# Optimization experiments

Measured on AMD Instinct MI355X. Metric: run time of the kernel, lower is better.

The kernel has to match this reference:

```python
import jax, jax.numpy as jnp
import numpy as np

V, B, NP, NJ = 5, 32, 20, 17
NB = 16
ND = 128
POSE_MIN_DEPTH, POSE_MAX_DEPTH = 2000.0, 8000.0
POSE_SIGMA = 100.0
KS = 11
HIDDEN_ROUGH, HIDDEN = 1024, 1024
BONES = np.array([[0,1],[0,2],[1,3],[2,4],[5,6],[5,7],[7,9],[6,8],[8,10],[5,11],[6,12],[11,12],[11,13],[13,15],[12,14],[14,16]], dtype=np.int32)


def setup_inputs() -> dict:
    key = jax.random.key(0)
    ks = jax.random.split(key, 12)
    wh = jnp.array([1920.0, 1080.0], jnp.float32)
    kpts = jax.random.uniform(ks[0], (V, B, NP, NJ, 2), jnp.float32) * wh
    pose_vis = jnp.ones((V, B, NP), jnp.float32)
    joint_vis = (jax.random.uniform(ks[1], (V, B, NP, NJ)) > 0.15).astype(jnp.float32)
    gt_pose_depths = jax.random.uniform(ks[2], (B, NP), jnp.float32, 2000.0, 8000.0)
    gt_joint_depths = jax.random.uniform(ks[3], (B, NP, NJ), jnp.float32, -100.0, 100.0)
    angles = np.linspace(-0.3, 0.3, V)
    Rs = np.stack([np.array([[np.cos(a), 0.0, np.sin(a)], [0.0, 1.0, 0.0], [-np.sin(a), 0.0, np.cos(a)]], dtype=np.float32) for a in angles])
    cam_R = jnp.broadcast_to(jnp.asarray(Rs)[:, None], (V, B, 3, 3))
    tvec = np.zeros((V, 3), np.float32); tvec[:, 0] = np.linspace(-500.0, 500.0, V)
    cam_T = jnp.broadcast_to(jnp.asarray(tvec)[:, None], (V, B, 3))
    cam_f = jnp.full((V, B, 2), 1400.0, jnp.float32)
    cam_c = jnp.broadcast_to(jnp.array([960.0, 540.0], jnp.float32), (V, B, 2))
    image_wh = jnp.broadcast_to(jnp.array([1920.0, 1080.0], jnp.float32), (V, B, 2))
    num_persons = jax.random.randint(ks[4], (V, B), 10, NP + 1, jnp.int32)
    Wr1 = jax.random.normal(ks[5], (HIDDEN_ROUGH, NJ * 2)) * 0.02
    br1 = jnp.zeros((HIDDEN_ROUGH,), jnp.float32)
    Wr2 = jax.random.normal(ks[6], (NJ, HIDDEN_ROUGH)) * 0.02
    br2 = jnp.zeros((NJ,), jnp.float32)
    Wc1 = jax.random.normal(ks[7], (HIDDEN, NJ + NB, 3)) * 0.02
    bc1 = jnp.zeros((HIDDEN,), jnp.float32)
    Wc2 = jax.random.normal(ks[8], (1, HIDDEN, 3)) * 0.02
    bc2 = jnp.zeros((1,), jnp.float32)
    bones = jnp.asarray(BONES)
    return dict(kpts=kpts, pose_vis=pose_vis, joint_vis=joint_vis, gt_pose_depths=gt_pose_depths, gt_joint_depths=gt_joint_depths, cam_R=cam_R, cam_T=cam_T, cam_f=cam_f, cam_c=cam_c, image_wh=image_wh, num_persons=num_persons, Wr1=Wr1, br1=br1, Wr2=Wr2, br2=br2, Wc1=Wc1, bc1=bc1, Wc2=Wc2, bc2=bc2, bones=bones)


def _bone_len(p, bones):
    # p: [B, Np, Nj, D, 2] -> [B, Np, Nb, D]
    a = p[:, :, bones[:, 0]]
    b = p[:, :, bones[:, 1]]
    return jnp.sqrt(jnp.sum((a - b) ** 2, -1) + 1e-12)


def _conv1d(x, w, b):
    # x [N,C,L], w [O,I,3]
    y = jax.lax.conv_general_dilated(x, w, (1,), 'SAME', dimension_numbers=('NCH', 'OIH', 'NCH'))
    return y + b[None, :, None]


def _forward(kpts, joint_vis, cam_R, cam_T, cam_f, cam_c, image_wh, num_persons, Wr1, br1, Wr2, br2, Wc1, bc1, Wc2, bc2, bones):
    V_, B_, NP_, NJ_, _ = kpts.shape
    labels = jnp.arange(ND, dtype=jnp.float32) / (ND - 1) * (POSE_MAX_DEPTH - POSE_MIN_DEPTH) + POSE_MIN_DEPTH
    kt = kpts[0]  # target-view 2D poses [B,Np,Nj,2]
    # faithful to original indexing quirk: normalize all batches by batch-0 image size
    kn = kt / image_wh[0, 0][None, None, None, :]
    x = kn.reshape(B_ * NP_, NJ_ * 2)
    h = jax.nn.relu(x @ Wr1.T + br1)
    rough = (h @ Wr2.T + br2).reshape(B_, NP_, NJ_) * 1000.0
    rough = jax.lax.stop_gradient(rough)  # .detach() in original
    depths = labels[None, None, None, :] + rough[..., None]  # [B,Np,Nj,D]
    # back-project target 2D poses at every depth hypothesis
    R0, T0, f0, c0 = cam_R[0], cam_T[0], cam_f[0], cam_c[0]
    uvn = (kt - c0[:, None, None, :]) / f0[:, None, None, :]
    xy = uvn[..., None, :] * depths[..., None]
    cam_pts = jnp.concatenate([xy, depths[..., None]], -1)
    p3d = jnp.einsum('bji,bpkdj->bpkdi', R0, cam_pts) + T0[:, None, None, None, :]  # world [B,Np,Nj,D,3]

    scores = scores2 = boundings = boundings2 = None
    for rv in range(1, V_):
        Rr, Tr, fr, cr = cam_R[rv], cam_T[rv], cam_f[rv], cam_c[rv]
        xc = jnp.einsum('bij,bpkdj->bpkdi', Rr, p3d - Tr[:, None, None, None, :])
        p2t = xc[..., :2] / (xc[..., 2:3] + 1e-8) * fr[:, None, None, None, :] + cr[:, None, None, None, :]
        pr = kpts[rv]         # [B,Npr,Nj,2]
        vr = joint_vis[rv]    # [B,Npr,Nj]
        # pairwise dist over (target-person, ref-person) per joint/depth
        d = jnp.sum((p2t[:, :, None] - pr[:, None, :, :, None, :]) ** 2, -1)  # [B,Npt,Npr,Nj,D]
        w = vr[:, None, :, :, None]
        pdist = jnp.sum(d * w, 3) / (jnp.sum(w, 3) + 1e-8)  # [B,Npt,Npr,D]
        valid = jnp.arange(NP_)[None, None, :, None] < num_persons[rv][:, None, None, None]
        pdist = jnp.where(valid, pdist, 1e5)
        mm = jnp.argmin(pdist, 2)  # [B,Npt,D] nearest ref pose
        bidx = jnp.arange(B_)[:, None, None]
        matched = jnp.transpose(pr[bidx, mm], (0, 1, 3, 2, 4))  # [B,Npt,Nj,D,2]
        mvis = jnp.transpose(vr[bidx, mm], (0, 1, 3, 2))        # [B,Npt,Nj,D]
        mdist = jnp.sum((p2t - matched) ** 2, -1)
        score = jnp.exp(-jnp.sqrt(mdist + 1e-12) / POSE_SIGMA)  # panoptic branch
        score_bl = jnp.exp(-jnp.abs(_bone_len(matched, bones) - _bone_len(p2t, bones)) / 5.0)
        wimg = image_wh[rv][:, None, None, None, 0]
        himg = image_wh[rv][:, None, None, None, 1]
        inb = ((p2t[..., 0] >= 0) & (p2t[..., 1] >= 0) & (p2t[..., 0] <= wimg - 1) & (p2t[..., 1] <= himg - 1)).astype(score.dtype)
        bounding = inb * mvis
        bounding2 = jnp.broadcast_to(mvis[:, :, :1, :], score_bl.shape)
        if scores is None:
            scores, scores2 = score * bounding, score_bl * bounding2
            boundings, boundings2 = bounding, bounding2
        else:
            scores = scores + score * bounding
            scores2 = scores2 + score_bl * bounding2
            boundings = boundings + bounding
            boundings2 = boundings2 + bounding2
    psv = (scores / (boundings + 1e-8)).reshape(B_ * NP_, NJ_, ND)
    psv2 = (scores2 / (boundings2 + 1e-8)).reshape(B_ * NP_, NB, ND)
    xin = jnp.concatenate([psv, psv2], 1)  # [BN, Nj+Nb, D]
    hc = jax.nn.relu(_conv1d(xin, Wc1, bc1))
    logits = _conv1d(hc, Wc2, bc2)[:, 0, :]  # [BN, D]
    vol = jax.nn.softmax(logits, -1)
    # soft-argmax restricted to a window around the argmax
    pos = jnp.arange(ND, dtype=vol.dtype)
    idx = jnp.argmax(vol, -1)
    mask = (jnp.abs(pos[None, :] - idx[:, None].astype(vol.dtype)) <= KS // 2).astype(vol.dtype)
    mv = vol * mask
    mv = mv / (jnp.sum(mv, -1, keepdims=True) + 1e-8)
    pred_idx = jnp.sum(mv * pos, -1).reshape(B_, NP_)
    return pred_idx / (ND - 1) * (POSE_MAX_DEPTH - POSE_MIN_DEPTH) + POSE_MIN_DEPTH


def reference(kpts, pose_vis, joint_vis, gt_pose_depths, gt_joint_depths, cam_R, cam_T, cam_f, cam_c, image_wh, num_persons, Wr1, br1, Wr2, br2, Wc1, bc1, Wc2, bc2, bones):
    return _forward(kpts, joint_vis, cam_R, cam_T, cam_f, cam_c, image_wh, num_persons, Wr1, br1, Wr2, br2, Wc1, bc1, Wc2, bc2, bones)
```

## Files before the change

kernel.cpp:

```cpp
#include <hip/hip_runtime.h>
#include <math.h>

#define VV  5
#define BB  32
#define NPP 20
#define NJJ 17
#define NBB 16
#define NDD 128
#define HID 1024
#define KPITCH 128
#define KSTEPS 7
#define PRP 36
#define VRP 20
#define NCH 34
#define RGH_P 20
#define BASE_P 52
#define A_T_ELEMS (32 * KSTEPS * 64 * 8)
#define EPI_ELEMS (32 * 4 * 64 * 16)

typedef __attribute__((ext_vector_type(8))) short short8;
typedef __attribute__((ext_vector_type(16))) float float16;

static constexpr int BONE_A[NBB] = {0,0,1,2,5,5,7,6,8,5,6,11,11,13,12,14};
static constexpr int BONE_B[NBB] = {1,2,3,4,6,7,9,8,10,11,12,12,13,15,14,16};

__device__ __forceinline__ float warp_red_sum(float v) {
#pragma unroll
  for (int off = 32; off >= 1; off >>= 1) v += __shfl_xor(v, off, 64);
  return v;
}

__global__ __launch_bounds__(256) void prep_kernel(
    const float* __restrict__ Wc1, const float* __restrict__ Wc2,
    const float* __restrict__ bc1,
    unsigned short* __restrict__ A_hi, unsigned short* __restrict__ A_lo,
    float* __restrict__ epi) {
  int gidx = blockIdx.x * 256 + threadIdx.x;
  if (gidx < A_T_ELEMS) {
    int e = gidx & 7;
    int l = (gidx >> 3) & 63;
    int rest = gidx >> 9;
    int ks = rest % 7;
    int ot = rest / 7;
    int o = ot * 32 + (l & 31);
    int kk = ks * 16 + (l >> 5) * 8 + e;
    float x = (kk < 99) ? Wc1[o * 99 + kk] : 0.0f;
    unsigned int u = __float_as_uint(x);
    unsigned short hi = (unsigned short)(u >> 16);
    float xh = __uint_as_float((u >> 16) << 16);
    unsigned short lo = (unsigned short)(__float_as_uint(x - xh) >> 16);
    A_hi[gidx] = hi;
    A_lo[gidx] = lo;
  } else {
    int idx2 = gidx - A_T_ELEMS;
    if (idx2 < EPI_ELEMS) {
      int c = idx2 & 15;
      int l = (idx2 >> 4) & 63;
      int rb = (idx2 >> 10) & 3;
      int ot = idx2 >> 12;
      int base = ot * 32 + 4 * (l >> 5) + 8 * rb;
      epi[idx2] = (c < 12) ? Wc2[base * 3 + c] : bc1[base + (c - 12)];
    }
  }
}

__global__ __launch_bounds__(256) void pose_pre_kernel(
    const float* __restrict__ kpts, const float* __restrict__ cam_R,
    const float* __restrict__ cam_f, const float* __restrict__ cam_c,
    const float* __restrict__ image_wh,
    const float* __restrict__ Wr1, const float* __restrict__ br1,
    const float* __restrict__ Wr2, const float* __restrict__ br2,
    float* __restrict__ ws_rough, float* __restrict__ ws_base) {
  const int n = blockIdx.x;
  const int b = n / NPP;
  const int p = n % NPP;
  const int tid = threadIdx.x;
  const int wv = tid >> 6, ln = tid & 63;

  __shared__ float sh_x[NJJ * 2];
  __shared__ float sh_h[HID];

  if (tid < NJJ * 2) {
    int j = tid >> 1, c = tid & 1;
    float k = kpts[((size_t)(b * NPP + p)) * NJJ * 2 + j * 2 + c];
    sh_x[tid] = k / image_wh[c];
  }
  __syncthreads();

#pragma unroll
  for (int k = 0; k < 4; ++k) {
    int m = tid + k * 256;
    float acc = br1[m];
#pragma unroll
    for (int c = 0; c < NJJ * 2; ++c) acc = fmaf(Wr1[m * (NJJ * 2) + c], sh_x[c], acc);
    sh_h[m] = fmaxf(acc, 0.0f);
  }
  __syncthreads();

  for (int j = wv; j < NJJ; j += 4) {
    float part = 0.0f;
    for (int m = ln; m < HID; m += 64) part = fmaf(Wr2[j * HID + m], sh_h[m], part);
    part = warp_red_sum(part);
    if (ln == 0) ws_rough[(size_t)n * RGH_P + j] = (part + br2[j]) * 1000.0f;
  }

  if (tid < NJJ) {
    int j = tid;
    const float* R0 = cam_R + (size_t)b * 9;
    float c0x = cam_c[b * 2 + 0], c0y = cam_c[b * 2 + 1];
    float f0x = cam_f[b * 2 + 0], f0y = cam_f[b * 2 + 1];
    float kx = kpts[((size_t)(b * NPP + p)) * NJJ * 2 + j * 2 + 0];
    float ky = kpts[((size_t)(b * NPP + p)) * NJJ * 2 + j * 2 + 1];
    float ux = (kx - c0x) / f0x;
    float uy = (ky - c0y) / f0y;
#pragma unroll
    for (int i = 0; i < 3; ++i)
      ws_base[(size_t)n * BASE_P + j * 3 + i] =
          R0[0 * 3 + i] * ux + R0[1 * 3 + i] * uy + R0[2 * 3 + i];
  }
}

__global__ __launch_bounds__(256, 4) void pose_match_kernel(
    const float* __restrict__ kpts, const float* __restrict__ joint_vis,
    const float* __restrict__ cam_R, const float* __restrict__ cam_T,
    const float* __restrict__ cam_f, const float* __restrict__ cam_c,
    const float* __restrict__ image_wh, const int* __restrict__ num_persons,
    const float* __restrict__ ws_rough, const float* __restrict__ ws_base,
    float* __restrict__ ws_partial) {
  const int bid = blockIdx.x;
  const int n = bid >> 1;
  const int bh = bid & 1;
  const int b = n / NPP;
  const int tid = threadIdx.x;
  const int rvv = tid >> 6;
  const int d = bh * 64 + (tid & 63);

  __shared__ float sh_rough[NJJ];
  __shared__ float sh_base[NJJ][3];
  __shared__ __align__(16) float sh_pr[4][NPP][PRP];
  __shared__ __align__(16) float sh_vr[4][NPP][VRP];

  if (tid < NJJ) sh_rough[tid] = ws_rough[(size_t)n * RGH_P + tid];
  if (tid >= 64 && tid < 64 + NJJ * 3)
    ((float*)sh_base)[tid - 64] = ws_base[(size_t)n * BASE_P + (tid - 64)];

#pragma unroll
  for (int rr = 0; rr < 4; ++rr) {
    const float* prg = kpts + ((size_t)(rr + 1) * BB + b) * NPP * NJJ * 2;
    for (int idx = tid; idx < NPP * NJJ * 2; idx += 256)
      sh_pr[rr][idx / 34][idx % 34] = prg[idx];
    const float* vrg = joint_vis + ((size_t)(rr + 1) * BB + b) * NPP * NJJ;
    for (int idx = tid; idx < NPP * NJJ; idx += 256)
      sh_vr[rr][idx / 17][idx % 17] = vrg[idx];
  }
  if (tid < 4 * BB) {
    int rr = tid >> 5, q = tid & 31;
    if (q < NPP) {
      sh_pr[rr][q][34] = 0.0f; sh_pr[rr][q][35] = 0.0f;
      sh_vr[rr][q][17] = 0.0f; sh_vr[rr][q][18] = 0.0f; sh_vr[rr][q][19] = 0.0f;
    }
  }
  __syncthreads();

  {
    const int rv = rvv + 1;
    const int vb = rv * BB + b;
    const float* Rr = cam_R + (size_t)vb * 9;
    const float R00 = Rr[0], R01 = Rr[1], R02 = Rr[2];
    const float R10 = Rr[3], R11 = Rr[4], R12 = Rr[5];
    const float R20 = Rr[6], R21 = Rr[7], R22 = Rr[8];
    const float Trx = cam_T[vb * 3 + 0], Try = cam_T[vb * 3 + 1], Trz = cam_T[vb * 3 + 2];
    const float frx = cam_f[vb * 2 + 0], fry = cam_f[vb * 2 + 1];
    const float crx = cam_c[vb * 2 + 0], cry = cam_c[vb * 2 + 1];
    const float wmax = image_wh[vb * 2 + 0] - 1.0f;
    const float hmax = image_wh[vb * 2 + 1] - 1.0f;
    const int nprv = num_persons[vb];
    const float T0x = cam_T[b * 3 + 0], T0y = cam_T[b * 3 + 1], T0z = cam_T[b * 3 + 2];
    const float lab = ((float)d / 127.0f) * 6000.0f + 2000.0f;

    float px[NJJ], py[NJJ];
#pragma unroll
    for (int j = 0; j < NJJ; ++j) {
      float dep = lab + sh_rough[j];
      float p0 = fmaf(dep, sh_base[j][0], T0x);
      float p1 = fmaf(dep, sh_base[j][1], T0y);
      float p2 = fmaf(dep, sh_base[j][2], T0z);
      float q0 = p0 - Trx, q1 = p1 - Try, q2 = p2 - Trz;
      float xc0 = R00 * q0 + R01 * q1 + R02 * q2;
      float xc1 = R10 * q0 + R11 * q1 + R12 * q2;
      float xc2 = R20 * q0 + R21 * q1 + R22 * q2 + 1e-8f;
      px[j] = xc0 / xc2 * frx + crx;
      py[j] = xc1 / xc2 * fry + cry;
    }

    float best = 3.4e38f;
    int mm = 0;
#pragma unroll 1
    for (int q = 0; q < NPP; ++q) {
      const float4* pr4 = (const float4*)(&sh_pr[rvv][q][0]);
      const float4* vr4 = (const float4*)(&sh_vr[rvv][q][0]);
      float num = 0.0f, den = 0.0f;
#pragma unroll
      for (int g4 = 0; g4 < 4; ++g4) {
        float4 w  = vr4[g4];
        float4 pa = pr4[2 * g4 + 0];
        float4 pb = pr4[2 * g4 + 1];
        { float dx = px[4*g4+0] - pa.x, dy = py[4*g4+0] - pa.y; num = fmaf(w.x, dx*dx + dy*dy, num); den += w.x; }
        { float dx = px[4*g4+1] - pa.z, dy = py[4*g4+1] - pa.w; num = fmaf(w.y, dx*dx + dy*dy, num); den += w.y; }
        { float dx = px[4*g4+2] - pb.x, dy = py[4*g4+2] - pb.y; num = fmaf(w.z, dx*dx + dy*dy, num); den += w.z; }
        { float dx = px[4*g4+3] - pb.z, dy = py[4*g4+3] - pb.w; num = fmaf(w.w, dx*dx + dy*dy, num); den += w.w; }
      }
      {
        float w16 = sh_vr[rvv][q][16];
        float4 pc = pr4[8];
        float dx = px[16] - pc.x, dy = py[16] - pc.y;
        num = fmaf(w16, dx*dx + dy*dy, num); den += w16;
      }
      float pd = num / (den + 1e-8f);
      if (q >= nprv) pd = 100000.0f;
      if (pd < best) { best = pd; mm = q; }
    }

    float* pbase = ws_partial + (((size_t)n * NCH) * 4 + rvv) * 128 + d;
    unsigned int maskB = 0u;
#pragma unroll
    for (int j = 0; j < NJJ; ++j) {
      float mx = sh_pr[rvv][mm][j * 2 + 0];
      float my = sh_pr[rvv][mm][j * 2 + 1];
      float mv = sh_vr[rvv][mm][j];
      float dx = px[j] - mx, dy = py[j] - my;
      float sc = expf(-sqrtf(dx * dx + dy * dy + 1e-12f) / 100.0f);
      float inb = (px[j] >= 0.0f && py[j] >= 0.0f && px[j] <= wmax && py[j] <= hmax) ? 1.0f : 0.0f;
      float bd = inb * mv;
      pbase[j * 512] = sc * bd;
      maskB |= ((unsigned int)(bd != 0.0f)) << j;
    }
    float v0 = sh_vr[rvv][mm][0];
    maskB |= ((unsigned int)(v0 != 0.0f)) << 17;
#pragma unroll
    for (int nb = 0; nb < NBB; ++nb) {
      const int a = BONE_A[nb], c = BONE_B[nb];
      float ax = sh_pr[rvv][mm][a * 2 + 0], ay = sh_pr[rvv][mm][a * 2 + 1];
      float cx = sh_pr[rvv][mm][c * 2 + 0], cy = sh_pr[rvv][mm][c * 2 + 1];
      float dmx = ax - cx, dmy = ay - cy;
      float blm = sqrtf(dmx * dmx + dmy * dmy + 1e-12f);
      float dpx = px[a] - px[c], dpy = py[a] - py[c];
      float blp = sqrtf(dpx * dpx + dpy * dpy + 1e-12f);
      float scb = expf(-fabsf(blm - blp) / 5.0f);
      pbase[(NJJ + nb) * 512] = scb * v0;
    }
    *(unsigned int*)(pbase + 33 * 512) = maskB;
  }
}

__global__ __launch_bounds__(128) void reduce_kernel(
    const float* __restrict__ ws_partial, float* __restrict__ ws_xin) {
  const int n = blockIdx.x;
  const int t = threadIdx.x;
  const float* pb = ws_partial + ((size_t)n * NCH) * 4 * 128;
  float* xo = ws_xin + (size_t)n * (NJJ + NBB) * NDD;

  unsigned int m0 = __float_as_uint(pb[(33 * 4 + 0) * 128 + t]);
  unsigned int m1 = __float_as_uint(pb[(33 * 4 + 1) * 128 + t]);
  unsigned int m2 = __float_as_uint(pb[(33 * 4 + 2) * 128 + t]);
  unsigned int m3 = __float_as_uint(pb[(33 * 4 + 3) * 128 + t]);

#pragma unroll
  for (int i = 0; i < NJJ; ++i) {
    const float* a = pb + (i * 4) * 128 + t;
    float s = ((a[0] + a[128]) + a[256]) + a[384];
    int bj = ((m0 >> i) & 1) + ((m1 >> i) & 1) + ((m2 >> i) & 1) + ((m3 >> i) & 1);
    xo[i * NDD + t] = s / ((float)bj + 1e-8f);
  }
  int b2 = ((m0 >> 17) & 1) + ((m1 >> 17) & 1) + ((m2 >> 17) & 1) + ((m3 >> 17) & 1);
  float den2 = (float)b2 + 1e-8f;
#pragma unroll
  for (int nb = 0; nb < NBB; ++nb) {
    const float* a = pb + ((NJJ + nb) * 4) * 128 + t;
    float s = ((a[0] + a[128]) + a[256]) + a[384];
    xo[(NJJ + nb) * NDD + t] = s / den2;
  }
}

__global__ __launch_bounds__(512, 2) void conv_mfma_kernel(
    const float* __restrict__ ws_xin,
    const unsigned short* __restrict__ A_hi, const unsigned short* __restrict__ A_lo,
    const float* __restrict__ epi,
    const float* __restrict__ bc2, float* __restrict__ out) {
  const int n = blockIdx.x;
  const int tid = threadIdx.x;
  const int w = tid >> 6;
  const int l = tid & 63;
  const int lrow = l & 31;
  const int g = l >> 5;

  __shared__ __align__(16) unsigned short bT_hi[128 * KPITCH];
  __shared__ __align__(16) unsigned short bT_lo[128 * KPITCH];
  __shared__ float plg[3][8][NDD];
  __shared__ float sh_l[NDD];
  __shared__ float sh_e[NDD];
  __shared__ float sh_sc[2];

  for (int i = tid; i < 3 * 8 * NDD; i += 512) ((float*)plg)[i] = 0.0f;

  const float* xn = ws_xin + (size_t)n * (NJJ + NBB) * NDD;
  for (int idx = tid; idx < 64 * 128; idx += 512) {
    const int kp = (idx & 63) << 1;
    const int t  = idx >> 6;
    unsigned int hp = 0, lp = 0;
#pragma unroll
    for (int u = 0; u < 2; ++u) {
      const int kk = kp + u;
      float x = 0.0f;
      if (kk < 99) {
        int i3 = kk / 3;
        int k3 = kk - i3 * 3;
        int tt = t + k3 - 1;
        if (tt >= 0 && tt < 128) x = xn[i3 * NDD + tt];
      }
      unsigned int uu = __float_as_uint(x);
      unsigned int hi = uu >> 16;
      float xh = __uint_as_float(hi << 16);
      unsigned int lo = __float_as_uint(x - xh) >> 16;
      hp |= hi << (16 * u);
      lp |= lo << (16 * u);
    }
    const int e = t * KPITCH + (kp ^ ((t & 15) << 3));
    *(unsigned int*)(bT_hi + e) = hp;
    *(unsigned int*)(bT_lo + e) = lp;
  }
  __syncthreads();

#pragma unroll 1
  for (int otile = 0; otile < 4; ++otile) {
    const int otg = w * 4 + otile;

    short8 Ah[KSTEPS], Al[KSTEPS];
    {
      const short8* ahT = ((const short8*)A_hi) + (size_t)otg * KSTEPS * 64 + l;
      const short8* alT = ((const short8*)A_lo) + (size_t)otg * KSTEPS * 64 + l;
#pragma unroll
      for (int ks = 0; ks < KSTEPS; ++ks) {
        Ah[ks] = ahT[ks * 64];
        Al[ks] = alT[ks * 64];
      }
    }
    float w2f[48];
    float bcf[16];
#pragma unroll
    for (int rb = 0; rb < 4; ++rb) {
      const float4* ep = ((const float4*)epi) + ((size_t)(otg * 4 + rb) * 64 + l) * 4;
      float4 e0 = ep[0], e1 = ep[1], e2 = ep[2], e3 = ep[3];
      w2f[rb * 12 + 0] = e0.x;  w2f[rb * 12 + 1] = e0.y;  w2f[rb * 12 + 2] = e0.z;
      w2f[rb * 12 + 3] = e0.w;  w2f[rb * 12 + 4] = e1.x;  w2f[rb * 12 + 5] = e1.y;
      w2f[rb * 12 + 6] = e1.z;  w2f[rb * 12 + 7] = e1.w;  w2f[rb * 12 + 8] = e2.x;
      w2f[rb * 12 + 9] = e2.y;  w2f[rb * 12 + 10] = e2.z; w2f[rb * 12 + 11] = e2.w;
      bcf[rb * 4 + 0] = e3.x; bcf[rb * 4 + 1] = e3.y;
      bcf[rb * 4 + 2] = e3.z; bcf[rb * 4 + 3] = e3.w;
    }

#pragma unroll 1
    for (int ttile = 0; ttile < 4; ++ttile) {
      const int trow = ttile * 32 + lrow;
      const unsigned short* brh = bT_hi + trow * KPITCH;
      const unsigned short* brl = bT_lo + trow * KPITCH;
      const int sw = (trow & 15) << 3;

      float16 X, Y;
#pragma unroll
      for (int r = 0; r < 16; ++r) { X[r] = 0.0f; Y[r] = 0.0f; }

#pragma unroll
      for (int ks = 0; ks < KSTEPS; ++ks) {
        const int e = (ks * 16 + g * 8) ^ sw;
        short8 bh8 = *(const short8*)(brh + e);
        X = __builtin_amdgcn_mfma_f32_32x32x16_bf16(Ah[ks], bh8, X, 0, 0, 0);
        Y = __builtin_amdgcn_mfma_f32_32x32x16_bf16(Al[ks], bh8, Y, 0, 0, 0);
      }
#pragma unroll
      for (int ks = 0; ks < KSTEPS; ++ks) {
        const int e = (ks * 16 + g * 8) ^ sw;
        short8 bl8 = *(const short8*)(brl + e);
        if (ks & 1) Y = __builtin_amdgcn_mfma_f32_32x32x16_bf16(Ah[ks], bl8, Y, 0, 0, 0);
        else        X = __builtin_amdgcn_mfma_f32_32x32x16_bf16(Ah[ks], bl8, X, 0, 0, 0);
      }

      float sP = 0.0f, sC = 0.0f, sM = 0.0f;
#pragma unroll
      for (int r = 0; r < 16; ++r) {
        float h = fmaxf((X[r] + Y[r]) + bcf[(r >> 2) * 4 + (r & 3)], 0.0f);
        sP = fmaf(h, w2f[(r >> 2) * 12 + (r & 3) * 3 + 0], sP);
        sC = fmaf(h, w2f[(r >> 2) * 12 + (r & 3) * 3 + 1], sC);
        sM = fmaf(h, w2f[(r >> 2) * 12 + (r & 3) * 3 + 2], sM);
      }
      sP += __shfl_xor(sP, 32, 64);
      sC += __shfl_xor(sC, 32, 64);
      sM += __shfl_xor(sM, 32, 64);
      if (l < 32) {
        plg[0][w][trow] += sP;
        plg[1][w][trow] += sC;
        plg[2][w][trow] += sM;
      }
    }
  }
  __syncthreads();

  if (tid < NDD) {
    int t = tid;
    float lg = bc2[0];
#pragma unroll
    for (int ww = 0; ww < 8; ++ww) lg += plg[1][ww][t];
    if (t > 0) {
#pragma unroll
      for (int ww = 0; ww < 8; ++ww) lg += plg[0][ww][t - 1];
    }
    if (t < NDD - 1) {
#pragma unroll
      for (int ww = 0; ww < 8; ++ww) lg += plg[2][ww][t + 1];
    }
    sh_l[t] = lg;
  }
  __syncthreads();
  if (tid < 64) {
    float v1 = sh_l[tid], v2 = sh_l[tid + 64];
    float mv; int mi;
    if (v2 > v1) { mv = v2; mi = tid + 64; } else { mv = v1; mi = tid; }
#pragma unroll
    for (int off = 32; off >= 1; off >>= 1) {
      float ov = __shfl_xor(mv, off, 64);
      int   oi = __shfl_xor(mi, off, 64);
      if (ov > mv || (ov == mv && oi < mi)) { mv = ov; mi = oi; }
    }
    if (tid == 0) { sh_sc[0] = mv; ((int*)sh_sc)[1] = mi; }
  }
  __syncthreads();
  const float gmax = sh_sc[0];
  const int gidx = ((const int*)sh_sc)[1];
  if (tid < NDD) sh_e[tid] = expf(sh_l[tid] - gmax);
  __syncthreads();
  if (tid < 64) {
    float S = warp_red_sum(sh_e[tid] + sh_e[tid + 64]);
    float a1 = 0.0f, a2 = 0.0f;
#pragma unroll
    for (int k = 0; k < 2; ++k) {
      int t = tid + k * 64;
      float vol = sh_e[t] / S;
      float msk = (fabsf((float)t - (float)gidx) <= 5.0f) ? 1.0f : 0.0f;
      float mvv = vol * msk;
      a1 += mvv;
      a2 += mvv * (float)t;
    }
    a1 = warp_red_sum(a1);
    a2 = warp_red_sum(a2);
    if (tid == 0) {
      float pred = a2 / (a1 + 1e-8f);
      out[n] = pred / 127.0f * 6000.0f + 2000.0f;
    }
  }
}

extern "C" void kernel_launch(void* const* d_in, const int* in_sizes, int n_in,
                              void* d_out, int out_size, void* d_ws, size_t ws_size,
                              hipStream_t stream) {
  (void)in_sizes; (void)n_in; (void)out_size; (void)ws_size;
  const float* kpts        = (const float*)d_in[0];
  const float* joint_vis   = (const float*)d_in[2];
  const float* cam_R       = (const float*)d_in[5];
  const float* cam_T       = (const float*)d_in[6];
  const float* cam_f       = (const float*)d_in[7];
  const float* cam_c       = (const float*)d_in[8];
  const float* image_wh    = (const float*)d_in[9];
  const int*   num_persons = (const int*)d_in[10];
  const float* Wr1 = (const float*)d_in[11];
  const float* br1 = (const float*)d_in[12];
  const float* Wr2 = (const float*)d_in[13];
  const float* br2 = (const float*)d_in[14];
  const float* Wc1 = (const float*)d_in[15];
  const float* bc1 = (const float*)d_in[16];
  const float* Wc2 = (const float*)d_in[17];
  const float* bc2 = (const float*)d_in[18];
  float* out = (float*)d_out;

  unsigned short* A_hi = (unsigned short*)d_ws;
  unsigned short* A_lo = A_hi + A_T_ELEMS;
  float* epi        = (float*)(A_lo + A_T_ELEMS);
  float* ws_xin     = epi + EPI_ELEMS;
  float* ws_partial = ws_xin + (size_t)BB * NPP * (NJJ + NBB) * NDD;
  float* ws_rough   = ws_partial + (size_t)BB * NPP * NCH * 4 * 128;
  float* ws_base    = ws_rough + (size_t)BB * NPP * RGH_P;

  const int prep_items = A_T_ELEMS + EPI_ELEMS;
  hipLaunchKernelGGL(prep_kernel, dim3((prep_items + 255) / 256), dim3(256), 0, stream,
                     Wc1, Wc2, bc1, A_hi, A_lo, epi);
  hipLaunchKernelGGL(pose_pre_kernel, dim3(BB * NPP), dim3(256), 0, stream,
                     kpts, cam_R, cam_f, cam_c, image_wh, Wr1, br1, Wr2, br2,
                     ws_rough, ws_base);
  hipLaunchKernelGGL(pose_match_kernel, dim3(BB * NPP * 2), dim3(256), 0, stream,
                     kpts, joint_vis, cam_R, cam_T, cam_f, cam_c, image_wh,
                     num_persons, ws_rough, ws_base, ws_partial);
  hipLaunchKernelGGL(reduce_kernel, dim3(BB * NPP), dim3(128), 0, stream,
                     ws_partial, ws_xin);
  hipLaunchKernelGGL(conv_mfma_kernel, dim3(BB * NPP), dim3(512), 0, stream,
                     ws_xin, A_hi, A_lo, epi, bc2, out);
}
```

Measured before the change: 188.8 us.

## Switch conv MFMA from 32x32x16 to 16x16x32 bf16 tiles

Replaces the 32x32x16 bf16 MFMA tiling of the first conv layer with 16x16x32 tiles. The weight pre-pack and epilogue (Wc2, bc1) layouts change to match, and K is padded to 128 (4 steps) instead of 112 (7 steps). Each wave now handles 8 output tiles of 16 channels, with two time tiles per pass and a shuffle reduction over 4 lane groups. The aim is to cut per-thread register pressure (4-wide accumulators instead of 16-wide) and use the K=32 instruction. The cost is wasted work on the extra zero padding in K and more shuffles and LDS accumulations in the epilogue.

Measured after the change: 193.9 us. 2.7% more time.

```diff
diff --git a/kernel.cpp b/kernel.cpp
--- a/kernel.cpp
+++ b/kernel.cpp
@@ -9,17 +9,16 @@
 #define NDD 128
 #define HID 1024
 #define KPITCH 128
-#define KSTEPS 7
 #define PRP 36
 #define VRP 20
 #define NCH 34
 #define RGH_P 20
 #define BASE_P 52
-#define A_T_ELEMS (32 * KSTEPS * 64 * 8)
-#define EPI_ELEMS (32 * 4 * 64 * 16)
+#define A2_ELEMS (64 * 4 * 64 * 8)
+#define EPI2_ELEMS (64 * 64 * 16)
 
 typedef __attribute__((ext_vector_type(8))) short short8;
-typedef __attribute__((ext_vector_type(16))) float float16;
+typedef __attribute__((ext_vector_type(4))) float floatx4;
 
 static constexpr int BONE_A[NBB] = {0,0,1,2,5,5,7,6,8,5,6,11,11,13,12,14};
 static constexpr int BONE_B[NBB] = {1,2,3,4,6,7,9,8,10,11,12,12,13,15,14,16};
@@ -36,14 +35,14 @@
     unsigned short* __restrict__ A_hi, unsigned short* __restrict__ A_lo,
     float* __restrict__ epi) {
   int gidx = blockIdx.x * 256 + threadIdx.x;
-  if (gidx < A_T_ELEMS) {
+  if (gidx < A2_ELEMS) {
     int e = gidx & 7;
     int l = (gidx >> 3) & 63;
     int rest = gidx >> 9;
-    int ks = rest % 7;
-    int ot = rest / 7;
-    int o = ot * 32 + (l & 31);
-    int kk = ks * 16 + (l >> 5) * 8 + e;
+    int ks = rest & 3;
+    int ot = rest >> 2;
+    int o = ot * 16 + (l & 15);
+    int kk = ks * 32 + (l >> 4) * 8 + e;
     float x = (kk < 99) ? Wc1[o * 99 + kk] : 0.0f;
     unsigned int u = __float_as_uint(x);
     unsigned short hi = (unsigned short)(u >> 16);
@@ -52,14 +51,13 @@
     A_hi[gidx] = hi;
     A_lo[gidx] = lo;
   } else {
-    int idx2 = gidx - A_T_ELEMS;
-    if (idx2 < EPI_ELEMS) {
+    int idx2 = gidx - A2_ELEMS;
+    if (idx2 < EPI2_ELEMS) {
       int c = idx2 & 15;
       int l = (idx2 >> 4) & 63;
-      int rb = (idx2 >> 10) & 3;
-      int ot = idx2 >> 12;
-      int base = ot * 32 + 4 * (l >> 5) + 8 * rb;
-      epi[idx2] = (c < 12) ? Wc2[base * 3 + c] : bc1[base + (c - 12)];
+      int ot = idx2 >> 10;
+      int base = ot * 16 + (l >> 4) * 4;
+      epi[idx2] = (c < 12) ? Wc2[(base + c / 3) * 3 + (c % 3)] : bc1[base + (c - 12)];
     }
   }
 }
@@ -291,8 +289,8 @@
   const int tid = threadIdx.x;
   const int w = tid >> 6;
   const int l = tid & 63;
-  const int lrow = l & 31;
-  const int g = l >> 5;
+  const int lcol = l & 15;
+  const int lg = l >> 4;
 
   __shared__ __align__(16) unsigned short bT_hi[128 * KPITCH];
   __shared__ __align__(16) unsigned short bT_lo[128 * KPITCH];
@@ -331,75 +329,104 @@
   }
   __syncthreads();
 
+  const int sw = lcol << 3;
+
 #pragma unroll 1
-  for (int otile = 0; otile < 4; ++otile) {
-    const int otg = w * 4 + otile;
-
-    short8 Ah[KSTEPS], Al[KSTEPS];
+  for (int oi = 0; oi < 8; ++oi) {
+    const int otg = w * 8 + oi;
+
+    short8 Ah[4], Al[4];
     {
-      const short8* ahT = ((const short8*)A_hi) + (size_t)otg * KSTEPS * 64 + l;
-      const short8* alT = ((const short8*)A_lo) + (size_t)otg * KSTEPS * 64 + l;
-#pragma unroll
-      for (int ks = 0; ks < KSTEPS; ++ks) {
+      const short8* ahT = ((const short8*)A_hi) + (size_t)otg * 4 * 64 + l;
+      const short8* alT = ((const short8*)A_lo) + (size_t)otg * 4 * 64 + l;
+#pragma unroll
+      for (int ks = 0; ks < 4; ++ks) {
         Ah[ks] = ahT[ks * 64];
         Al[ks] = alT[ks * 64];
       }
     }
-    float w2f[48];
-    float bcf[16];
-#pragma unroll
-    for (int rb = 0; rb < 4; ++rb) {
-      const float4* ep = ((const float4*)epi) + ((size_t)(otg * 4 + rb) * 64 + l) * 4;
+    float w2f[12];
+    float bcf[4];
+    {
+      const float4* ep = ((const float4*)epi) + ((size_t)otg * 64 + l) * 4;
       float4 e0 = ep[0], e1 = ep[1], e2 = ep[2], e3 = ep[3];
-      w2f[rb * 12 + 0] = e0.x;  w2f[rb * 12 + 1] = e0.y;  w2f[rb * 12 + 2] = e0.z;
-      w2f[rb * 12 + 3] = e0.w;  w2f[rb * 12 + 4] = e1.x;  w2f[rb * 12 + 5] = e1.y;
-      w2f[rb * 12 + 6] = e1.z;  w2f[rb * 12 + 7] = e1.w;  w2f[rb * 12 + 8] = e2.x;
-      w2f[rb * 12 + 9] = e2.y;  w2f[rb * 12 + 10] = e2.z; w2f[rb * 12 + 11] = e2.w;
-      bcf[rb * 4 + 0] = e3.x; bcf[rb * 4 + 1] = e3.y;
-      bcf[rb * 4 + 2] = e3.z; bcf[rb * 4 + 3] = e3.w;
+      w2f[0] = e0.x; w2f[1] = e0.y; w2f[2] = e0.z; w2f[3] = e0.w;
+      w2f[4] = e1.x; w2f[5] = e1.y; w2f[6] = e1.z; w2f[7] = e1.w;
+      w2f[8] = e2.x; w2f[9] = e2.y; w2f[10] = e2.z; w2f[11] = e2.w;
+      bcf[0] = e3.x; bcf[1] = e3.y; bcf[2] = e3.z; bcf[3] = e3.w;
     }
 
 #pragma unroll 1
-    for (int ttile = 0; ttile < 4; ++ttile) {
-      const int trow = ttile * 32 + lrow;
-      const unsigned short* brh = bT_hi + trow * KPITCH;
-      const unsigned short* brl = bT_lo + trow * KPITCH;
-      const int sw = (trow & 15) << 3;
-
-      float16 X, Y;
-#pragma unroll
-      for (int r = 0; r < 16; ++r) { X[r] = 0.0f; Y[r] = 0.0f; }
-
-#pragma unroll
-      for (int ks = 0; ks < KSTEPS; ++ks) {
-        const int e = (ks * 16 + g * 8) ^ sw;
-        short8 bh8 = *(const short8*)(brh + e);
-        X = __builtin_amdgcn_mfma_f32_32x32x16_bf16(Ah[ks], bh8, X, 0, 0, 0);
-        Y = __builtin_amdgcn_mfma_f32_32x32x16_bf16(Al[ks], bh8, Y, 0, 0, 0);
-      }
-#pragma unroll
-      for (int ks = 0; ks < KSTEPS; ++ks) {
-        const int e = (ks * 16 + g * 8) ^ sw;
-        short8 bl8 = *(const short8*)(brl + e);
-        if (ks & 1) Y = __builtin_amdgcn_mfma_f32_32x32x16_bf16(Ah[ks], bl8, Y, 0, 0, 0);
-        else        X = __builtin_amdgcn_mfma_f32_32x32x16_bf16(Ah[ks], bl8, X, 0, 0, 0);
-      }
-
-      float sP = 0.0f, sC = 0.0f, sM = 0.0f;
-#pragma unroll
-      for (int r = 0; r < 16; ++r) {
-        float h = fmaxf((X[r] + Y[r]) + bcf[(r >> 2) * 4 + (r & 3)], 0.0f);
-        sP = fmaf(h, w2f[(r >> 2) * 12 + (r & 3) * 3 + 0], sP);
-        sC = fmaf(h, w2f[(r >> 2) * 12 + (r & 3) * 3 + 1], sC);
-        sM = fmaf(h, w2f[(r >> 2) * 12 + (r & 3) * 3 + 2], sM);
-      }
-      sP += __shfl_xor(sP, 32, 64);
-      sC += __shfl_xor(sC, 32, 64);
-      sM += __shfl_xor(sM, 32, 64);
-      if (l < 32) {
-        plg[0][w][trow] += sP;
-        plg[1][w][trow] += sC;
-        plg[2][w][trow] += sM;
+    for (int tp = 0; tp < 4; ++tp) {
+      const int t0 = tp * 32 + lcol;
+      const int t1 = t0 + 16;
+      const unsigned short* b0h = bT_hi + t0 * KPITCH;
+      const unsigned short* b1h = bT_hi + t1 * KPITCH;
+      const unsigned short* b0l = bT_lo + t0 * KPITCH;
+      const unsigned short* b1l = bT_lo + t1 * KPITCH;
+
+      floatx4 X0 = {0.f, 0.f, 0.f, 0.f}, Y0 = {0.f, 0.f, 0.f, 0.f};
+      floatx4 X1 = {0.f, 0.f, 0.f, 0.f}, Y1 = {0.f, 0.f, 0.f, 0.f};
+
+#pragma unroll
+      for (int ks = 0; ks < 4; ++ks) {
+        const int e = (ks * 32 + lg * 8) ^ sw;
+        short8 bh0 = *(const short8*)(b0h + e);
+        short8 bh1 = *(const short8*)(b1h + e);
+        X0 = __builtin_amdgcn_mfma_f32_16x16x32_bf16(Ah[ks], bh0, X0, 0, 0, 0);
+        Y0 = __builtin_amdgcn_mfma_f32_16x16x32_bf16(Al[ks], bh0, Y0, 0, 0, 0);
+        X1 = __builtin_amdgcn_mfma_f32_16x16x32_bf16(Ah[ks], bh1, X1, 0, 0, 0);
+        Y1 = __builtin_amdgcn_mfma_f32_16x16x32_bf16(Al[ks], bh1, Y1, 0, 0, 0);
+      }
+#pragma unroll
+      for (int ks = 0; ks < 4; ++ks) {
+        const int e = (ks * 32 + lg * 8) ^ sw;
+        short8 bl0 = *(const short8*)(b0l + e);
+        short8 bl1 = *(const short8*)(b1l + e);
+        if (ks & 1) {
+          Y0 = __builtin_amdgcn_mfma_f32_16x16x32_bf16(Ah[ks], bl0, Y0, 0, 0, 0);
+          Y1 = __builtin_amdgcn_mfma_f32_16x16x32_bf16(Ah[ks], bl1, Y1, 0, 0, 0);
+        } else {
+          X0 = __builtin_amdgcn_mfma_f32_16x16x32_bf16(Ah[ks], bl0, X0, 0, 0, 0);
+          X1 = __builtin_amdgcn_mfma_f32_16x16x32_bf16(Ah[ks], bl1, X1, 0, 0, 0);
+        }
+      }
+
+      {
+        float sP = 0.0f, sC = 0.0f, sM = 0.0f;
+#pragma unroll
+        for (int r = 0; r < 4; ++r) {
+          float h = fmaxf((X0[r] + Y0[r]) + bcf[r], 0.0f);
+          sP = fmaf(h, w2f[r * 3 + 0], sP);
+          sC = fmaf(h, w2f[r * 3 + 1], sC);
+          sM = fmaf(h, w2f[r * 3 + 2], sM);
+        }
+        sP += __shfl_xor(sP, 16, 64); sP += __shfl_xor(sP, 32, 64);
+        sC += __shfl_xor(sC, 16, 64); sC += __shfl_xor(sC, 32, 64);
+        sM += __shfl_xor(sM, 16, 64); sM += __shfl_xor(sM, 32, 64);
+        if (lg == 0) {
+          plg[0][w][t0] += sP;
+          plg[1][w][t0] += sC;
+          plg[2][w][t0] += sM;
+        }
+      }
+      {
+        float sP = 0.0f, sC = 0.0f, sM = 0.0f;
+#pragma unroll
+        for (int r = 0; r < 4; ++r) {
+          float h = fmaxf((X1[r] + Y1[r]) + bcf[r], 0.0f);
+          sP = fmaf(h, w2f[r * 3 + 0], sP);
+          sC = fmaf(h, w2f[r * 3 + 1], sC);
+          sM = fmaf(h, w2f[r * 3 + 2], sM);
+        }
+        sP += __shfl_xor(sP, 16, 64); sP += __shfl_xor(sP, 32, 64);
+        sC += __shfl_xor(sC, 16, 64); sC += __shfl_xor(sC, 32, 64);
+        sM += __shfl_xor(sM, 16, 64); sM += __shfl_xor(sM, 32, 64);
+        if (lg == 0) {
+          plg[0][w][t1] += sP;
+          plg[1][w][t1] += sC;
+          plg[2][w][t1] += sM;
+        }
       }
     }
   }
@@ -407,18 +434,18 @@
 
   if (tid < NDD) {
     int t = tid;
-    float lg = bc2[0];
-#pragma unroll
-    for (int ww = 0; ww < 8; ++ww) lg += plg[1][ww][t];
+    float lg2 = bc2[0];
+#pragma unroll
+    for (int ww = 0; ww < 8; ++ww) lg2 += plg[1][ww][t];
     if (t > 0) {
 #pragma unroll
-      for (int ww = 0; ww < 8; ++ww) lg += plg[0][ww][t - 1];
+      for (int ww = 0; ww < 8; ++ww) lg2 += plg[0][ww][t - 1];
     }
     if (t < NDD - 1) {
 #pragma unroll
-      for (int ww = 0; ww < 8; ++ww) lg += plg[2][ww][t + 1];
-    }
-    sh_l[t] = lg;
+      for (int ww = 0; ww < 8; ++ww) lg2 += plg[2][ww][t + 1];
+    }
+    sh_l[t] = lg2;
   }
   __syncthreads();
   if (tid < 64) {
@@ -428,8 +455,8 @@
 #pragma unroll
     for (int off = 32; off >= 1; off >>= 1) {
       float ov = __shfl_xor(mv, off, 64);
-      int   oi = __shfl_xor(mi, off, 64);
-      if (ov > mv || (ov == mv && oi < mi)) { mv = ov; mi = oi; }
+      int   oi2 = __shfl_xor(mi, off, 64);
+      if (ov > mv || (ov == mv && oi2 < mi)) { mv = ov; mi = oi2; }
     }
     if (tid == 0) { sh_sc[0] = mv; ((int*)sh_sc)[1] = mi; }
   }
@@ -482,14 +509,14 @@
   float* out = (float*)d_out;
 
   unsigned short* A_hi = (unsigned short*)d_ws;
-  unsigned short* A_lo = A_hi + A_T_ELEMS;
-  float* epi        = (float*)(A_lo + A_T_ELEMS);
-  float* ws_xin     = epi + EPI_ELEMS;
+  unsigned short* A_lo = A_hi + A2_ELEMS;
+  float* epi        = (float*)(A_lo + A2_ELEMS);
+  float* ws_xin     = epi + EPI2_ELEMS;
   float* ws_partial = ws_xin + (size_t)BB * NPP * (NJJ + NBB) * NDD;
   float* ws_rough   = ws_partial + (size_t)BB * NPP * NCH * 4 * 128;
   float* ws_base    = ws_rough + (size_t)BB * NPP * RGH_P;
 
-  const int prep_items = A_T_ELEMS + EPI_ELEMS;
+  const int prep_items = A2_ELEMS + EPI2_ELEMS;
   hipLaunchKernelGGL(prep_kernel, dim3((prep_items + 255) / 256), dim3(256), 0, stream,
                      Wc1, Wc2, bc1, A_hi, A_lo, epi);
   hipLaunchKernelGGL(pose_pre_kernel, dim3(BB * NPP), dim3(256), 0, stream,
```
